# Optimization experiments

Measured on AMD Instinct MI355X. Metric: run time of the kernel, lower is better.

Reference implementation:

```python
import jax, jax.numpy as jnp
import numpy as np

ALPHA = 0.2  # LeakyReLU negative slope
V_NODES = 7  # fixed by the module (self.B, self.A are 7x7)


def setup_inputs() -> dict:
    key = jax.random.key(0)
    k1, k2, k3 = jax.random.split(key, 3)
    N, C, T, V = 64, 256, 256, V_NODES
    F = 256  # out_features
    h = jax.random.normal(k1, (N, C, T, V), dtype=jnp.float32)
    # xavier_uniform with gain=1.414 ~ U(-b, b), b = gain*sqrt(6/(fan_in+fan_out))
    bW = 1.414 * np.sqrt(6.0 / (T + F))
    W = jax.random.uniform(k2, (T, F), dtype=jnp.float32, minval=-bW, maxval=bW)
    ba = 1.414 * np.sqrt(6.0 / (2 * F + 1))
    a = jax.random.uniform(k3, (2 * F, 1), dtype=jnp.float32, minval=-ba, maxval=ba)
    B = jnp.zeros((V, V), dtype=jnp.float32) + 1e-6
    return {"h": h, "W": W, "a": a, "B": B}


def reference(h, W, a, B):
    # h: (N, C, T, V) -> (N, V, C, T)
    h = jnp.transpose(h, (0, 3, 1, 2))
    Wh = jnp.matmul(h, W)                       # (N, V, C, F)
    F = Wh.shape[-1]
    a1 = a[:F, 0]                               # (F,)
    a2 = a[F:, 0]                               # (F,)
    # e[n,i,j,c] = a1.Wh[n,i,c,:] + a2.Wh[n,j,c,:]  (avoids (N,V,V,C,2F) materialization)
    s1 = jnp.einsum('nicf,f->nic', Wh, a1)      # (N, V, C)
    s2 = jnp.einsum('njcf,f->njc', Wh, a2)      # (N, V, C)
    e = s1[:, :, None, :] + s2[:, None, :, :]   # (N, V, V, C)
    e = jnp.where(e > 0, e, ALPHA * e)          # LeakyReLU
    att = jax.nn.softmax(e, axis=-1)            # softmax over channel dim C
    # normalized adjacency: min-max then symmetric degree normalization
    V_ = B.shape[0]
    adj = B + jnp.eye(V_, dtype=B.dtype)
    adj = (adj - jnp.min(adj)) / (jnp.max(adj) - jnp.min(adj))
    d_inv_sqrt = 1.0 / jnp.sqrt(jnp.sum(adj, axis=1))
    adj_norm = adj * d_inv_sqrt[:, None] * d_inv_sqrt[None, :]
    # diag_embed(att) matmul loop == channel-wise weighted sum over j
    h_agg = jnp.einsum('njcf,nijc->nicf', Wh, att)        # (N, V, C, F)
    out = jnp.einsum('nicf,iv->ncfv', h_agg, adj_norm)    # (N, C, F, V)
    return jax.nn.elu(out)
```

## Files before the change

kernel.cpp:

```cpp
#include <hip/hip_runtime.h>
#include <hip/hip_bf16.h>

#define LRELU_ALPHA 0.2f

typedef __attribute__((ext_vector_type(8))) short short8;
typedef __attribute__((ext_vector_type(4))) float f32x4;

__device__ __forceinline__ float bf2f(unsigned short u) {
  union { unsigned int i; float f; } x;
  x.i = ((unsigned int)u) << 16;
  return x.f;
}

__global__ __launch_bounds__(256) void k0_wt(const float* __restrict__ W,
                                             __hip_bfloat16* __restrict__ Wt) {
  int t = blockIdx.x, f = threadIdx.x;
  Wt[f * 256 + t] = __float2bfloat16(W[t * 256 + f]);
}

__global__ __launch_bounds__(64) void k0_wa(const float* __restrict__ W,
                                            const float* __restrict__ a,
                                            float* __restrict__ Wa) {
  int t = blockIdx.x, lane = threadIdx.x;
  float4 wv = *reinterpret_cast<const float4*>(W + t * 256 + lane * 4);
  float4 a1 = *reinterpret_cast<const float4*>(a + lane * 4);
  float4 a2 = *reinterpret_cast<const float4*>(a + 256 + lane * 4);
  float p1 = wv.x * a1.x + wv.y * a1.y + wv.z * a1.z + wv.w * a1.w;
  float p2 = wv.x * a2.x + wv.y * a2.y + wv.z * a2.z + wv.w * a2.w;
  #pragma unroll
  for (int off = 32; off; off >>= 1) {
    p1 += __shfl_down(p1, off);
    p2 += __shfl_down(p2, off);
  }
  if (lane == 0) { Wa[t] = p1; Wa[256 + t] = p2; }
}

__global__ __launch_bounds__(64) void k0_adj(const float* __restrict__ B,
                                             float* __restrict__ adjn) {
  int t = threadIdx.x;
  float v = 0.f;
  if (t < 49) v = B[t] + (((t / 7) == (t % 7)) ? 1.f : 0.f);
  float mn = (t < 49) ? v : 1e30f;
  float mx = (t < 49) ? v : -1e30f;
  #pragma unroll
  for (int off = 32; off; off >>= 1) {
    mn = fminf(mn, __shfl_xor(mn, off));
    mx = fmaxf(mx, __shfl_xor(mx, off));
  }
  float scaled = (v - mn) / (mx - mn);
  __shared__ float adj[49];
  __shared__ float dis[7];
  if (t < 49) adj[t] = scaled;
  __syncthreads();
  if (t < 7) {
    float s = 0.f;
    #pragma unroll
    for (int j = 0; j < 7; ++j) s += adj[t * 7 + j];
    dis[t] = 1.0f / sqrtf(s);
  }
  __syncthreads();
  if (t < 49) adjn[t] = adj[t] * dis[t / 7] * dis[t % 7];
}

__global__ __launch_bounds__(256, 4) void k1_gemm(const float* __restrict__ h,
                                                  const __hip_bfloat16* __restrict__ Wt,
                                                  const float* __restrict__ Wa,
                                                  __hip_bfloat16* __restrict__ Wh,
                                                  float* __restrict__ s1g,
                                                  float* __restrict__ s2g) {
  __shared__ __hip_bfloat16 As[56][264];
  const int blk = blockIdx.x;
  const int n = blk >> 5, cb = blk & 31;
  const int tid = threadIdx.x;

  const float4* src =
      reinterpret_cast<const float4*>(h + (size_t)(n * 256 + cb * 8) * 1792);
  #pragma unroll
  for (int it = 0; it < 14; ++it) {
    int idx4 = tid + it * 256;
    float4 val = src[idx4];
    int base = idx4 * 4;
    const float* vp = reinterpret_cast<const float*>(&val);
    #pragma unroll
    for (int q = 0; q < 4; ++q) {
      int idx = base + q;
      int c = idx / 1792;
      int r = idx - c * 1792;
      int t = r / 7;
      int v = r - t * 7;
      As[c * 7 + v][t] = __float2bfloat16(vp[q]);
    }
  }
  __syncthreads();

  const int lane = tid & 63, wave = tid >> 6;
  const int lr = lane & 15, lk = lane >> 4;
  const int f_base = wave * 64;

  f32x4 acc[4][4];
  #pragma unroll
  for (int mt = 0; mt < 4; ++mt)
    #pragma unroll
    for (int ft = 0; ft < 4; ++ft) acc[mt][ft] = (f32x4){0.f, 0.f, 0.f, 0.f};

  const short* WtS = reinterpret_cast<const short*>(Wt);
  const short* AsS = reinterpret_cast<const short*>(&As[0][0]);

  int rowm[4];
  #pragma unroll
  for (int mt = 0; mt < 4; ++mt) {
    int m = mt * 16 + lr;
    rowm[mt] = (m < 56) ? m : 55;
  }

  for (int k0 = 0; k0 < 256; k0 += 32) {
    short8 b[4];
    #pragma unroll
    for (int ft = 0; ft < 4; ++ft)
      b[ft] = *reinterpret_cast<const short8*>(
          WtS + (f_base + ft * 16 + lr) * 256 + k0 + lk * 8);
    #pragma unroll
    for (int mt = 0; mt < 4; ++mt) {
      short8 afrag = *reinterpret_cast<const short8*>(
          AsS + rowm[mt] * 264 + k0 + lk * 8);
      #pragma unroll
      for (int ft = 0; ft < 4; ++ft)
        acc[mt][ft] = __builtin_amdgcn_mfma_f32_16x16x32_bf16(afrag, b[ft],
                                                              acc[mt][ft], 0, 0, 0);
    }
  }

  #pragma unroll
  for (int mt = 0; mt < 4; ++mt) {
    #pragma unroll
    for (int j = 0; j < 4; ++j) {
      int m = mt * 16 + lk * 4 + j;
      if (m < 56) {
        int cl = m / 7;
        int v = m - cl * 7;
        __hip_bfloat16* dst =
            Wh + (size_t)((n * 256 + cb * 8 + cl) * 7 + v) * 256 + f_base + lr;
        #pragma unroll
        for (int ft = 0; ft < 4; ++ft)
          dst[ft * 16] = __float2bfloat16(acc[mt][ft][j]);
      }
    }
  }

  const int gid = tid >> 4;
  const int fl = tid & 15;
  float wa1[16], wa2[16];
  #pragma unroll
  for (int q = 0; q < 16; ++q) {
    wa1[q] = Wa[fl * 16 + q];
    wa2[q] = Wa[256 + fl * 16 + q];
  }
  #pragma unroll
  for (int k = 0; k < 4; ++k) {
    int m = k * 16 + gid;
    if (m < 56) {
      short8 r0 = *reinterpret_cast<const short8*>(AsS + m * 264 + fl * 16);
      short8 r1 = *reinterpret_cast<const short8*>(AsS + m * 264 + fl * 16 + 8);
      float p1 = 0.f, p2 = 0.f;
      #pragma unroll
      for (int q = 0; q < 8; ++q) {
        float x = bf2f((unsigned short)r0[q]);
        p1 += x * wa1[q];
        p2 += x * wa2[q];
        float y = bf2f((unsigned short)r1[q]);
        p1 += y * wa1[8 + q];
        p2 += y * wa2[8 + q];
      }
      #pragma unroll
      for (int off = 1; off <= 8; off <<= 1) {
        p1 += __shfl_xor(p1, off);
        p2 += __shfl_xor(p2, off);
      }
      if (fl == 0) {
        int cl = m / 7, v = m - cl * 7;
        int c = cb * 8 + cl;
        s1g[(n * 7 + v) * 256 + c] = p1;
        s2g[(n * 7 + v) * 256 + c] = p2;
      }
    }
  }
}

__global__ __launch_bounds__(256) void k2_soft(const float* __restrict__ s1g,
                                               const float* __restrict__ s2g,
                                               float* __restrict__ att) {
  __shared__ float s1L[1792], s2L[1792];
  const int n = blockIdx.x, tid = threadIdx.x;
  for (int idx = tid; idx < 1792; idx += 256) {
    s1L[idx] = s1g[n * 1792 + idx];
    s2L[idx] = s2g[n * 1792 + idx];
  }
  __syncthreads();
  const int lane = tid & 63, wave = tid >> 6;
  for (int p = wave; p < 49; p += 4) {
    int i = p / 7, j = p - i * 7;
    float ex[4];
    float mx = -1e30f;
    #pragma unroll
    for (int q = 0; q < 4; ++q) {
      int c = lane + q * 64;
      float e = s1L[i * 256 + c] + s2L[j * 256 + c];
      e = (e > 0.f) ? e : LRELU_ALPHA * e;
      ex[q] = e;
      mx = fmaxf(mx, e);
    }
    #pragma unroll
    for (int off = 32; off; off >>= 1) mx = fmaxf(mx, __shfl_xor(mx, off));
    float sm = 0.f;
    #pragma unroll
    for (int q = 0; q < 4; ++q) {
      ex[q] = __expf(ex[q] - mx);
      sm += ex[q];
    }
    #pragma unroll
    for (int off = 32; off; off >>= 1) sm += __shfl_xor(sm, off);
    float inv = 1.0f / sm;
    #pragma unroll
    for (int q = 0; q < 4; ++q) {
      int c = lane + q * 64;
      att[((size_t)n * 256 + c) * 49 + p] = ex[q] * inv;
    }
  }
}

__global__ __launch_bounds__(256) void k3_out(const __hip_bfloat16* __restrict__ Wh,
                                              const float* __restrict__ att,
                                              const float* __restrict__ adjn,
                                              float* __restrict__ out) {
  __shared__ float attL[49], adjL[49], M[49];
  __shared__ float outL[1792];
  const int blk = blockIdx.x;
  const int n = blk >> 8, c = blk & 255;
  const int tid = threadIdx.x;
  if (tid < 49) {
    attL[tid] = att[((size_t)n * 256 + c) * 49 + tid];
    adjL[tid] = adjn[tid];
  }
  __syncthreads();
  if (tid < 49) {
    int j = tid / 7, v = tid - (tid / 7) * 7;
    float s = 0.f;
    #pragma unroll
    for (int i = 0; i < 7; ++i) s += attL[i * 7 + j] * adjL[i * 7 + v];
    M[tid] = s;
  }
  __syncthreads();
  const unsigned short* WhS = reinterpret_cast<const unsigned short*>(Wh) +
                              ((size_t)n * 256 + c) * 1792 + tid;
  float wh[7];
  #pragma unroll
  for (int j = 0; j < 7; ++j) wh[j] = bf2f(WhS[j * 256]);
  #pragma unroll
  for (int v = 0; v < 7; ++v) {
    float o = 0.f;
    #pragma unroll
    for (int j = 0; j < 7; ++j) o += wh[j] * M[j * 7 + v];
    o = (o > 0.f) ? o : (__expf(o) - 1.f);
    outL[tid * 7 + v] = o;
  }
  __syncthreads();
  float* dst = out + (size_t)(n * 256 + c) * 1792;
  for (int idx = tid; idx < 1792; idx += 256) dst[idx] = outL[idx];
}

extern "C" void kernel_launch(void* const* d_in, const int* in_sizes, int n_in,
                              void* d_out, int out_size, void* d_ws, size_t ws_size,
                              hipStream_t stream) {
  const float* h = (const float*)d_in[0];
  const float* W = (const float*)d_in[1];
  const float* a = (const float*)d_in[2];
  const float* B = (const float*)d_in[3];
  float* out = (float*)d_out;
  char* ws = (char*)d_ws;

  __hip_bfloat16* Wt = (__hip_bfloat16*)(ws + 0);
  float* adjn = (float*)(ws + 131072);
  float* Wa   = (float*)(ws + 131328);
  float* s1g  = (float*)(ws + 133376);
  float* s2g  = (float*)(ws + 592128);
  float* att  = (float*)(ws + 1050880);
  __hip_bfloat16* Wh = (__hip_bfloat16*)(ws + 4262144);

  k0_wt<<<256, 256, 0, stream>>>(W, Wt);
  k0_wa<<<256, 64, 0, stream>>>(W, a, Wa);
  k0_adj<<<1, 64, 0, stream>>>(B, adjn);
  k1_gemm<<<2048, 256, 0, stream>>>(h, Wt, Wa, Wh, s1g, s2g);
  k2_soft<<<64, 256, 0, stream>>>(s1g, s2g, att);
  k3_out<<<16384, 256, 0, stream>>>(Wh, att, adjn, out);
}
```

Before: 115.7 us.

## Stage W tiles through LDS with register prefetch in GEMM kernel

The GEMM kernel now loads all of its h input into registers before the LDS transpose, and stages the Wt operand in a padded shared-memory tile. The next K-slice of Wt is prefetched into registers while the MFMAs for the current slice run. This replaces per-wave direct global loads of B fragments with cooperative coalesced loads, and hides some of their latency. In exchange the kernel adds two barriers per K step, uses more LDS, and drops the occupancy hint from launch_bounds, so register pressure could lower occupancy.

```diff
diff --git a/kernel.cpp b/kernel.cpp
--- a/kernel.cpp
+++ b/kernel.cpp
@@ -62,25 +62,43 @@
   if (t < 49) adjn[t] = adj[t] * dis[t / 7] * dis[t % 7];
 }
 
-__global__ __launch_bounds__(256, 4) void k1_gemm(const float* __restrict__ h,
-                                                  const __hip_bfloat16* __restrict__ Wt,
-                                                  const float* __restrict__ Wa,
-                                                  __hip_bfloat16* __restrict__ Wh,
-                                                  float* __restrict__ s1g,
-                                                  float* __restrict__ s2g) {
+__global__ __launch_bounds__(256) void k1_gemm(const float* __restrict__ h,
+                                               const __hip_bfloat16* __restrict__ Wt,
+                                               const float* __restrict__ Wa,
+                                               __hip_bfloat16* __restrict__ Wh,
+                                               float* __restrict__ s1g,
+                                               float* __restrict__ s2g) {
   __shared__ __hip_bfloat16 As[56][264];
+  __shared__ short BsS[256 * 40];
   const int blk = blockIdx.x;
   const int n = blk >> 5, cb = blk & 31;
   const int tid = threadIdx.x;
 
+  const short* WtS = reinterpret_cast<const short*>(Wt);
+
+  int bf[4], bkc[4];
+  #pragma unroll
+  for (int it = 0; it < 4; ++it) {
+    int idx16 = tid + it * 256;
+    bf[it] = idx16 >> 2;
+    bkc[it] = idx16 & 3;
+  }
+
   const float4* src =
       reinterpret_cast<const float4*>(h + (size_t)(n * 256 + cb * 8) * 1792);
+  float4 vals[14];
+  #pragma unroll
+  for (int it = 0; it < 14; ++it) vals[it] = src[tid + it * 256];
+
+  short8 breg[4];
+  #pragma unroll
+  for (int it = 0; it < 4; ++it)
+    breg[it] = *reinterpret_cast<const short8*>(WtS + bf[it] * 256 + bkc[it] * 8);
+
   #pragma unroll
   for (int it = 0; it < 14; ++it) {
-    int idx4 = tid + it * 256;
-    float4 val = src[idx4];
-    int base = idx4 * 4;
-    const float* vp = reinterpret_cast<const float*>(&val);
+    int base = (tid + it * 256) * 4;
+    const float* vp = reinterpret_cast<const float*>(&vals[it]);
     #pragma unroll
     for (int q = 0; q < 4; ++q) {
       int idx = base + q;
@@ -91,6 +109,9 @@
       As[c * 7 + v][t] = __float2bfloat16(vp[q]);
     }
   }
+  #pragma unroll
+  for (int it = 0; it < 4; ++it)
+    *reinterpret_cast<short8*>(BsS + bf[it] * 40 + bkc[it] * 8) = breg[it];
   __syncthreads();
 
   const int lane = tid & 63, wave = tid >> 6;
@@ -103,7 +124,6 @@
     #pragma unroll
     for (int ft = 0; ft < 4; ++ft) acc[mt][ft] = (f32x4){0.f, 0.f, 0.f, 0.f};
 
-  const short* WtS = reinterpret_cast<const short*>(Wt);
   const short* AsS = reinterpret_cast<const short*>(&As[0][0]);
 
   int rowm[4];
@@ -113,20 +133,35 @@
     rowm[mt] = (m < 56) ? m : 55;
   }
 
-  for (int k0 = 0; k0 < 256; k0 += 32) {
-    short8 b[4];
+  #pragma unroll
+  for (int kb = 0; kb < 8; ++kb) {
+    short8 bnext[4];
+    if (kb < 7) {
+      #pragma unroll
+      for (int it = 0; it < 4; ++it)
+        bnext[it] = *reinterpret_cast<const short8*>(
+            WtS + bf[it] * 256 + (kb + 1) * 32 + bkc[it] * 8);
+    }
+    short8 bfrag[4];
     #pragma unroll
     for (int ft = 0; ft < 4; ++ft)
-      b[ft] = *reinterpret_cast<const short8*>(
-          WtS + (f_base + ft * 16 + lr) * 256 + k0 + lk * 8);
+      bfrag[ft] = *reinterpret_cast<const short8*>(
+          BsS + (f_base + ft * 16 + lr) * 40 + lk * 8);
     #pragma unroll
     for (int mt = 0; mt < 4; ++mt) {
       short8 afrag = *reinterpret_cast<const short8*>(
-          AsS + rowm[mt] * 264 + k0 + lk * 8);
+          AsS + rowm[mt] * 264 + kb * 32 + lk * 8);
       #pragma unroll
       for (int ft = 0; ft < 4; ++ft)
-        acc[mt][ft] = __builtin_amdgcn_mfma_f32_16x16x32_bf16(afrag, b[ft],
+        acc[mt][ft] = __builtin_amdgcn_mfma_f32_16x16x32_bf16(afrag, bfrag[ft],
                                                               acc[mt][ft], 0, 0, 0);
+    }
+    __syncthreads();
+    if (kb < 7) {
+      #pragma unroll
+      for (int it = 0; it < 4; ++it)
+        *reinterpret_cast<short8*>(BsS + bf[it] * 40 + bkc[it] * 8) = bnext[it];
+      __syncthreads();
     }
   }
 
```

New measurement: 111.1 us. -4.0%, faster.
